# Kernel optimization log

Hardware: AMD Instinct MI355X
Metric: run time of the kernel (lower is better)

## Reference

```python
import jax, jax.numpy as jnp
import numpy as np

POOL = 7
IMG_H, IMG_W = 1024, 1024
EPS = 1e-3  # keras BatchNormalization default epsilon


def crop_and_resize(fmap, boxes, ph, pw):
    # TF tf.image.crop_and_resize (bilinear), box_indices == batch index of each roi.
    # fmap: [B,H,W,C], boxes: [B,N,4] normalized (y1,x1,y2,x2) -> [B,N,ph,pw,C]
    B, H, W, C = fmap.shape
    y1, x1, y2, x2 = jnp.split(boxes, 4, axis=-1)  # each [B,N,1]
    fy = jnp.arange(ph, dtype=boxes.dtype) / (ph - 1)
    fx = jnp.arange(pw, dtype=boxes.dtype) / (pw - 1)
    ys = (y1 + (y2 - y1) * fy) * (H - 1)  # [B,N,ph]
    xs = (x1 + (x2 - x1) * fx) * (W - 1)  # [B,N,pw]
    y0 = jnp.floor(ys)
    x0 = jnp.floor(xs)
    wy = (ys - y0)[:, :, :, None, None]  # [B,N,ph,1,1]
    wx = (xs - x0)[:, :, None, :, None]  # [B,N,1,pw,1]
    y0i = jnp.clip(y0.astype(jnp.int32), 0, H - 1)
    y1i = jnp.clip(y0i + 1, 0, H - 1)
    x0i = jnp.clip(x0.astype(jnp.int32), 0, W - 1)
    x1i = jnp.clip(x0i + 1, 0, W - 1)
    b = jnp.arange(B)[:, None, None, None]
    yi0 = y0i[:, :, :, None]; yi1 = y1i[:, :, :, None]   # [B,N,ph,1]
    xi0 = x0i[:, :, None, :]; xi1 = x1i[:, :, None, :]   # [B,N,1,pw]
    v00 = fmap[b, yi0, xi0]  # [B,N,ph,pw,C]
    v01 = fmap[b, yi0, xi1]
    v10 = fmap[b, yi1, xi0]
    v11 = fmap[b, yi1, xi1]
    top = v00 + (v01 - v00) * wx
    bot = v10 + (v11 - v10) * wx
    return top + (bot - top) * wy


def pyramid_roi_align(rois, fmaps, pool):
    # rois are stop-gradient in the original layer
    rois = jax.lax.stop_gradient(rois)
    y1, x1, y2, x2 = jnp.split(rois, 4, axis=-1)
    h = y2 - y1
    w = x2 - x1
    scale = 256.0 / np.sqrt(float(IMG_H * IMG_W))
    lvl = jnp.log2(jnp.maximum(jnp.sqrt(h * w), 1e-9) / scale)
    lvl = jnp.clip(4 + jnp.round(lvl).astype(jnp.int32), 2, 5)[..., 0]  # [B,N]
    B, N = rois.shape[:2]
    C = fmaps[0].shape[-1]
    out = jnp.zeros((B, N, pool, pool, C), fmaps[0].dtype)
    for i, fm in enumerate(fmaps):  # levels 2..5, fixed small loop
        sel = (lvl == i + 2)[:, :, None, None, None]
        out = jnp.where(sel, crop_and_resize(fm, rois, pool, pool), out)
    return out


def bn_train(x, gamma, beta):
    # keras BatchNorm with training=True: biased batch stats over all axes but channel
    m = x.mean(axis=(0, 1))
    v = x.var(axis=(0, 1))
    return (x - m) * jax.lax.rsqrt(v + EPS) * gamma + beta


def setup_inputs() -> dict:
    key = jax.random.key(0)
    ks = jax.random.split(key, 12)
    B, N, C, F = 2, 1000, 256, 1024
    # rois: valid boxes, sizes spanning all pyramid levels
    tl = jax.random.uniform(ks[0], (B, N, 2), jnp.float32, 0.0, 0.6)
    sz = jax.random.uniform(ks[1], (B, N, 2), jnp.float32, 0.02, 0.4)
    br = jnp.minimum(tl + sz, 1.0)
    rois = jnp.concatenate([tl[..., :1], tl[..., 1:], br[..., :1], br[..., 1:]], axis=-1)
    s = 0.02
    return {
        "rois": rois,
        "p2": jax.random.normal(ks[2], (B, 256, 256, C), jnp.float32),
        "p3": jax.random.normal(ks[3], (B, 128, 128, C), jnp.float32),
        "p4": jax.random.normal(ks[4], (B, 64, 64, C), jnp.float32),
        "p5": jax.random.normal(ks[5], (B, 32, 32, C), jnp.float32),
        "conv1_w": jax.random.normal(ks[6], (POOL, POOL, C, F), jnp.float32) * s,
        "conv1_b": jnp.zeros((F,), jnp.float32),
        "bn1_g": jnp.ones((F,), jnp.float32),
        "bn1_b": jnp.zeros((F,), jnp.float32),
        "conv2_w": jax.random.normal(ks[7], (F, F), jnp.float32) * s,
        "conv2_b": jnp.zeros((F,), jnp.float32),
        "bn2_g": jnp.ones((F,), jnp.float32),
        "bn2_b": jnp.zeros((F,), jnp.float32),
        "cls_w": jax.random.normal(ks[8], (F, 2), jnp.float32) * s,
        "cls_b": jnp.zeros((2,), jnp.float32),
        "delta_w": jax.random.normal(ks[9], (F, 8), jnp.float32) * s,
        "delta_b": jnp.zeros((8,), jnp.float32),
    }


def reference(rois, p2, p3, p4, p5, conv1_w, conv1_b, bn1_g, bn1_b,
              conv2_w, conv2_b, bn2_g, bn2_b, cls_w, cls_b, delta_w, delta_b):
    B, N = rois.shape[:2]
    n_classes = cls_w.shape[-1]
    pooled = pyramid_roi_align(rois, (p2, p3, p4, p5), POOL)  # [B,N,7,7,C]
    # Conv2D(F,(7,7),'valid') on a 7x7 input == full contraction over (h,w,c)
    x = jnp.einsum('bnhwc,hwcf->bnf', pooled, conv1_w) + conv1_b
    x = jax.nn.relu(bn_train(x, bn1_g, bn1_b))
    x = x @ conv2_w + conv2_b  # 1x1 conv == dense
    shared = jax.nn.relu(bn_train(x, bn2_g, bn2_b))  # [B,N,F]
    logits = shared @ cls_w + cls_b                  # [B,N,n_classes]
    probs = jax.nn.softmax(logits, axis=-1)
    deltas = (shared @ delta_w + delta_b).reshape(B, N, n_classes, 4)
    return logits, probs, deltas
```

## Files before the change

kernel.cpp:

```cpp
#include <hip/hip_runtime.h>
#include <hip/hip_bf16.h>

#define NB     2
#define NROI   1000
#define CIN    256
#define FDIM   1024
#define M_ROWS 2000
#define K1     12544
#define EPSBN  1e-3f
#define MN     (M_ROWS * FDIM)

typedef short bf16x8 __attribute__((ext_vector_type(8)));
typedef float f32x4  __attribute__((ext_vector_type(4)));

__device__ __forceinline__ void gld_lds16(const void* g, void* l) {
  __builtin_amdgcn_global_load_lds((const __attribute__((address_space(1))) char*)g,
                                   (__attribute__((address_space(3))) char*)l, 16, 0, 0);
}

__global__ void transpose_to_bf16(const float* __restrict__ W,
                                  __hip_bfloat16* __restrict__ WT,
                                  int K, int N) {
  __shared__ float tile[32][33];
  int k0 = blockIdx.x * 32, n0 = blockIdx.y * 32;
  int t = threadIdx.x;
  int j = t & 31;
  for (int i = t >> 5; i < 32; i += 8)
    tile[i][j] = W[(size_t)(k0 + i) * N + n0 + j];
  __syncthreads();
  int k = t & 31;
  for (int n = t >> 5; n < 32; n += 8)
    WT[(size_t)(n0 + n) * K + k0 + k] = __float2bfloat16(tile[k][n]);
}

__global__ void roi_align_kernel(const float* __restrict__ rois,
                                 const float* __restrict__ p2,
                                 const float* __restrict__ p3,
                                 const float* __restrict__ p4,
                                 const float* __restrict__ p5,
                                 __hip_bfloat16* __restrict__ pooled) {
  int idx = blockIdx.x;
  int pos = idx % 49;
  int rn  = idx / 49;
  int n = rn % NROI, b = rn / NROI;
  int py = pos / 7, px = pos % 7;

  const float* roi = rois + (size_t)(b * NROI + n) * 4;
  float y1 = roi[0], x1 = roi[1], y2 = roi[2], x2 = roi[3];
  float h = y2 - y1, w = x2 - x1;
  float lvl = log2f(fmaxf(sqrtf(h * w), 1e-9f) * 4.0f);
  int li = 4 + (int)rintf(lvl);
  li = min(max(li, 2), 5) - 2;

  const float* fm; int H;
  switch (li) {
    case 0:  fm = p2; H = 256; break;
    case 1:  fm = p3; H = 128; break;
    case 2:  fm = p4; H = 64;  break;
    default: fm = p5; H = 32;  break;
  }
  int W = H;

  float fy = (float)py / 6.0f, fx = (float)px / 6.0f;
  float ys = (y1 + (y2 - y1) * fy) * (float)(H - 1);
  float xs = (x1 + (x2 - x1) * fx) * (float)(W - 1);
  float y0f = floorf(ys), x0f = floorf(xs);
  float wy = ys - y0f, wx = xs - x0f;
  int y0 = min(max((int)y0f, 0), H - 1);
  int x0 = min(max((int)x0f, 0), W - 1);
  int y1i = min(y0 + 1, H - 1);
  int x1i = min(x0 + 1, W - 1);

  size_t base = (size_t)b * H * W * CIN;
  const float* p00 = fm + base + ((size_t)y0 * W + x0) * CIN;
  const float* p01 = fm + base + ((size_t)y0 * W + x1i) * CIN;
  const float* p10 = fm + base + ((size_t)y1i * W + x0) * CIN;
  const float* p11 = fm + base + ((size_t)y1i * W + x1i) * CIN;

  int c = threadIdx.x;
  float v00 = p00[c], v01 = p01[c], v10 = p10[c], v11 = p11[c];
  float top = v00 + (v01 - v00) * wx;
  float bot = v10 + (v11 - v10) * wx;
  float val = top + (bot - top) * wy;
  pooled[(size_t)idx * CIN + c] = __float2bfloat16(val);
}

template<int KSLICES>
__global__ __launch_bounds__(256) void gemm128(const short* __restrict__ A,
                                               const short* __restrict__ BT,
                                               float* __restrict__ P,
                                               int M, int N, int K) {
  __shared__ short As[128 * 32];
  __shared__ short Bs[128 * 32];

  int nwg = gridDim.x;
  int bid = blockIdx.x;
  int cpx = nwg >> 3;
  int wg = (bid & 7) * cpx + (bid >> 3);

  int MT = (M + 127) >> 7;
  int NT = N >> 7;
  int ks   = wg / (MT * NT);
  int tile = wg % (MT * NT);
  int tm = tile % MT, tn = tile / MT;
  int m0 = tm * 128, n0 = tn * 128;
  int Kc = K / KSLICES;
  int kb = ks * Kc;

  int t = threadIdx.x;
  int lane = t & 63, wid = t >> 6;
  int wr = wid >> 1, wc = wid & 1;

  int q0 = wid * 64 + lane;
  int q1 = 256 + q0;
  int as0 = (q0 & 3) * 8, as1 = (q1 & 3) * 8;
  int ar0 = min(m0 + (q0 >> 2), M - 1);
  int ar1 = min(m0 + (q1 >> 2), M - 1);
  const short* Ag0 = A + (size_t)ar0 * K + kb + as0;
  const short* Ag1 = A + (size_t)ar1 * K + kb + as1;
  const short* Bg0 = BT + (size_t)(n0 + (q0 >> 2)) * K + kb + as0;
  const short* Bg1 = BT + (size_t)(n0 + (q1 >> 2)) * K + kb + as1;
  short* Asb0 = As + wid * 512;
  short* Asb1 = As + 2048 + wid * 512;
  short* Bsb0 = Bs + wid * 512;
  short* Bsb1 = Bs + 2048 + wid * 512;

  int lrow = lane & 15, lk = (lane >> 4) * 8;
  const short* Ar = As + (wr * 64 + lrow) * 32 + lk;
  const short* Br = Bs + (wc * 64 + lrow) * 32 + lk;

  f32x4 acc[4][4] = {};

  for (int k0 = 0; k0 < Kc; k0 += 32) {
    __syncthreads();
    gld_lds16(Ag0 + k0, Asb0);
    gld_lds16(Ag1 + k0, Asb1);
    gld_lds16(Bg0 + k0, Bsb0);
    gld_lds16(Bg1 + k0, Bsb1);
    __syncthreads();

    bf16x8 af[4], bfr[4];
#pragma unroll
    for (int i = 0; i < 4; i++) {
      af[i]  = *(const bf16x8*)(Ar + i * 512);
      bfr[i] = *(const bf16x8*)(Br + i * 512);
    }
#pragma unroll
    for (int mi = 0; mi < 4; mi++)
#pragma unroll
      for (int ni = 0; ni < 4; ni++)
        acc[mi][ni] = __builtin_amdgcn_mfma_f32_16x16x32_bf16(af[mi], bfr[ni], acc[mi][ni], 0, 0, 0);
  }

  float* Pb = P + (size_t)ks * M * N;
  int crow = (lane >> 4) * 4, ccol = lane & 15;
#pragma unroll
  for (int mi = 0; mi < 4; mi++) {
    int rb = m0 + wr * 64 + mi * 16 + crow;
#pragma unroll
    for (int ni = 0; ni < 4; ni++) {
      int col = n0 + wc * 64 + ni * 16 + ccol;
#pragma unroll
      for (int r = 0; r < 4; r++) {
        int row = rb + r;
        if (row < M) Pb[(size_t)row * N + col] = acc[mi][ni][r];
      }
    }
  }
}

template<int KS>
__global__ void reduce_bias(const float* __restrict__ P, const float* __restrict__ bias,
                            float* __restrict__ X, int mn, int N) {
  int i4 = blockIdx.x * blockDim.x + threadIdx.x;
  if (i4 * 4 >= mn) return;
  f32x4 s = *(const f32x4*)(P + (size_t)i4 * 4);
#pragma unroll
  for (int c = 1; c < KS; c++)
    s = s + *(const f32x4*)(P + (size_t)c * mn + i4 * 4);
  int col = (i4 * 4) & (N - 1);
  s = s + *(const f32x4*)(bias + col);
  *(f32x4*)(X + (size_t)i4 * 4) = s;
}

__global__ void bn_stats(const float* __restrict__ X, float* __restrict__ stats, int M) {
  int t = threadIdx.x;
  float s0 = 0, s1 = 0, s2 = 0, s3 = 0;
  float q0 = 0, q1 = 0, q2 = 0, q3 = 0;
  for (int r = blockIdx.x; r < M; r += gridDim.x) {
    const float* row = X + (size_t)r * FDIM;
    float v0 = row[t], v1 = row[t + 256], v2 = row[t + 512], v3 = row[t + 768];
    s0 += v0; s1 += v1; s2 += v2; s3 += v3;
    q0 += v0 * v0; q1 += v1 * v1; q2 += v2 * v2; q3 += v3 * v3;
  }
  atomicAdd(&stats[t], s0);        atomicAdd(&stats[t + 256], s1);
  atomicAdd(&stats[t + 512], s2);  atomicAdd(&stats[t + 768], s3);
  atomicAdd(&stats[FDIM + t], q0);       atomicAdd(&stats[FDIM + t + 256], q1);
  atomicAdd(&stats[FDIM + t + 512], q2); atomicAdd(&stats[FDIM + t + 768], q3);
}

template <bool BF16OUT>
__global__ void bn_norm_relu(const float* __restrict__ X, const float* __restrict__ stats,
                             const float* __restrict__ g, const float* __restrict__ bta,
                             __hip_bfloat16* __restrict__ obf, float* __restrict__ of32,
                             int M) {
  int idx = blockIdx.x * blockDim.x + threadIdx.x;
  if (idx >= M * FDIM) return;
  int f = idx & (FDIM - 1);
  float inv_m = 1.0f / (float)M;
  float mean = stats[f] * inv_m;
  float var = stats[FDIM + f] * inv_m - mean * mean;
  float xn = (X[idx] - mean) * rsqrtf(var + EPSBN) * g[f] + bta[f];
  xn = fmaxf(xn, 0.0f);
  if (BF16OUT) obf[idx] = __float2bfloat16(xn);
  else         of32[idx] = xn;
}

__global__ void heads_kernel(const float* __restrict__ S,
                             const float* __restrict__ cls_w, const float* __restrict__ cls_b,
                             const float* __restrict__ dw, const float* __restrict__ db,
                             float* __restrict__ out) {
  int row = blockIdx.x * 4 + (threadIdx.x >> 6);
  int lane = threadIdx.x & 63;
  if (row >= M_ROWS) return;
  const float* srow = S + (size_t)row * FDIM;
  float a[10];
#pragma unroll
  for (int j = 0; j < 10; j++) a[j] = 0.0f;
  for (int k = lane; k < FDIM; k += 64) {
    float v = srow[k];
    a[0] += v * cls_w[k * 2 + 0];
    a[1] += v * cls_w[k * 2 + 1];
#pragma unroll
    for (int j = 0; j < 8; j++) a[2 + j] += v * dw[k * 8 + j];
  }
#pragma unroll
  for (int j = 0; j < 10; j++)
    for (int o = 32; o > 0; o >>= 1) a[j] += __shfl_xor(a[j], o, 64);
  if (lane == 0) {
    float l0 = a[0] + cls_b[0], l1 = a[1] + cls_b[1];
    out[row * 2 + 0] = l0;
    out[row * 2 + 1] = l1;
    float mx = fmaxf(l0, l1);
    float e0 = expf(l0 - mx), e1 = expf(l1 - mx);
    float inv = 1.0f / (e0 + e1);
    out[4000 + row * 2 + 0] = e0 * inv;
    out[4000 + row * 2 + 1] = e1 * inv;
#pragma unroll
    for (int j = 0; j < 8; j++) out[8000 + row * 8 + j] = a[2 + j] + db[j];
  }
}

extern "C" void kernel_launch(void* const* d_in, const int* in_sizes, int n_in,
                              void* d_out, int out_size, void* d_ws, size_t ws_size,
                              hipStream_t stream) {
  const float* rois    = (const float*)d_in[0];
  const float* p2      = (const float*)d_in[1];
  const float* p3      = (const float*)d_in[2];
  const float* p4      = (const float*)d_in[3];
  const float* p5      = (const float*)d_in[4];
  const float* conv1_w = (const float*)d_in[5];
  const float* conv1_b = (const float*)d_in[6];
  const float* bn1_g   = (const float*)d_in[7];
  const float* bn1_b   = (const float*)d_in[8];
  const float* conv2_w = (const float*)d_in[9];
  const float* conv2_b = (const float*)d_in[10];
  const float* bn2_g   = (const float*)d_in[11];
  const float* bn2_b   = (const float*)d_in[12];
  const float* cls_w   = (const float*)d_in[13];
  const float* cls_b   = (const float*)d_in[14];
  const float* delta_w = (const float*)d_in[15];
  const float* delta_b = (const float*)d_in[16];
  float* out = (float*)d_out;

  char* ws = (char*)d_ws;
  size_t off = 0;
  __hip_bfloat16* pooled = (__hip_bfloat16*)(ws + off); off += (size_t)M_ROWS * K1 * 2;
  __hip_bfloat16* w1t    = (__hip_bfloat16*)(ws + off); off += (size_t)K1 * FDIM * 2;
  __hip_bfloat16* w2t    = (__hip_bfloat16*)(ws + off); off += (size_t)FDIM * FDIM * 2;
  float* x1              = (float*)(ws + off);          off += (size_t)MN * 4;
  float* stats1          = (float*)(ws + off);          off += 2 * FDIM * 4;
  float* stats2          = (float*)(ws + off);          off += 2 * FDIM * 4;
  char*  Preg            = ws + off;                    off += (size_t)4 * MN * 4;
  float* part1           = (float*)Preg;
  __hip_bfloat16* x1n    = (__hip_bfloat16*)Preg;
  float* x2              = (float*)(Preg + (size_t)MN * 4);
  float* shared_f        = (float*)(Preg + (size_t)2 * MN * 4);

  hipMemsetAsync(stats1, 0, 4 * FDIM * sizeof(float), stream);

  transpose_to_bf16<<<dim3(K1 / 32, FDIM / 32), 256, 0, stream>>>(conv1_w, w1t, K1, FDIM);
  transpose_to_bf16<<<dim3(FDIM / 32, FDIM / 32), 256, 0, stream>>>(conv2_w, w2t, FDIM, FDIM);

  roi_align_kernel<<<NB * NROI * 49, CIN, 0, stream>>>(rois, p2, p3, p4, p5, pooled);

  gemm128<4><<<512, 256, 0, stream>>>((const short*)pooled, (const short*)w1t, part1,
                                      M_ROWS, FDIM, K1);
  reduce_bias<4><<<MN / 1024, 256, 0, stream>>>(part1, conv1_b, x1, MN, FDIM);

  bn_stats<<<400, 256, 0, stream>>>(x1, stats1, M_ROWS);
  bn_norm_relu<true><<<(MN + 255) / 256, 256, 0, stream>>>(
      x1, stats1, bn1_g, bn1_b, x1n, nullptr, M_ROWS);

  gemm128<2><<<256, 256, 0, stream>>>((const short*)x1n, (const short*)w2t, x2,
                                      M_ROWS, FDIM, FDIM);
  reduce_bias<2><<<MN / 1024, 256, 0, stream>>>(x2, conv2_b, x2, MN, FDIM);

  bn_stats<<<400, 256, 0, stream>>>(x2, stats2, M_ROWS);
  bn_norm_relu<false><<<(MN + 255) / 256, 256, 0, stream>>>(
      x2, stats2, bn2_g, bn2_b, nullptr, shared_f, M_ROWS);

  heads_kernel<<<(M_ROWS + 3) / 4, 256, 0, stream>>>(shared_f, cls_w, cls_b, delta_w, delta_b, out);

  (void)in_sizes; (void)n_in; (void)out_size; (void)ws_size;
}
```

Before: 256.8 us.

## Add 8-wave pipelined GEMM and fuse split-K reduce with BN stats and heads

Replaces the first-layer GEMM with a 512-thread kernel. It uses 128x256 tiles, a multi-buffered global-to-LDS async load pipeline with explicit waitcnt and barrier scheduling, and raised priority for the MFMA section. The split-K reduction and bias add are fused with the batch-norm statistics accumulation. The second batch-norm and ReLU are folded into the heads kernel, which removes the intermediate shared-feature buffer. Workspace buffers are aliased more aggressively, which reorders the second weight transpose, and the larger LDS footprint may limit occupancy.

```diff
diff --git a/kernel.cpp b/kernel.cpp
--- a/kernel.cpp
+++ b/kernel.cpp
@@ -86,13 +86,121 @@
 }
 
 template<int KSLICES>
+__global__ __launch_bounds__(512) void gemm8w(const short* __restrict__ A,
+                                              const short* __restrict__ BT,
+                                              float* __restrict__ P,
+                                              int M, int N, int K) {
+  __shared__ short As[4 * 128 * 32];
+  __shared__ short Bs[4 * 256 * 32];
+
+  int nwg = gridDim.x;
+  int bid = blockIdx.x;
+  int cpx = nwg >> 3;
+  int wg = (bid & 7) * cpx + (bid >> 3);
+
+  int MT = (M + 127) >> 7;
+  int NTn = N >> 8;
+  int tiles = MT * NTn;
+  int ks = wg / tiles;
+  int rem = wg % tiles;
+  int tm = rem % MT, tn = rem / MT;
+  int m0 = tm * 128, n0 = tn * 256;
+  int Kc = K / KSLICES;
+  int NT = Kc >> 6;
+  size_t kb = (size_t)ks * Kc;
+
+  int tid = threadIdx.x;
+  int lane = tid & 63, wid = tid >> 6;
+  int wr = wid >> 2, wc = wid & 3;
+
+  int srow = tid >> 2;
+  int g = (tid & 3) ^ (srow & 3);
+  const short* Agb  = A  + (size_t)min(m0 + srow, M - 1) * K + kb + g * 8;
+  const short* Bgb0 = BT + (size_t)(n0 + srow) * K + kb + g * 8;
+  const short* Bgb1 = Bgb0 + (size_t)128 * K;
+  int aoff  = wid * 512;
+  int boff0 = wid * 512;
+  int boff1 = 4096 + wid * 512;
+
+  int lr = lane & 15;
+  int slotoff = ((lane >> 4) ^ (lane & 3)) * 8;
+  const short* Ard = As + (wr * 64 + lr) * 32 + slotoff;
+  const short* Brd = Bs + (wc * 64 + lr) * 32 + slotoff;
+
+  f32x4 acc[4][4] = {};
+
+#define STAGE(s) do {                                                        \
+    int ts_ = (s) >> 1, kh_ = (s) & 1, b_ = ts_ & 1;                         \
+    int ko_ = ts_ * 64 + kh_ * 32;                                           \
+    short* Ad_ = (short*)As + (b_ * 2 + kh_) * 4096 + aoff;                  \
+    short* Bd_ = (short*)Bs + (b_ * 2 + kh_) * 8192;                         \
+    gld_lds16(Agb + ko_, Ad_);                                               \
+    gld_lds16(Bgb0 + ko_, Bd_ + boff0);                                      \
+    gld_lds16(Bgb1 + ko_, Bd_ + boff1);                                      \
+  } while (0)
+
+  STAGE(0); STAGE(1); STAGE(2);
+
+  for (int t = 0; t < NT; ++t) {
+    int b = t & 1;
+#pragma unroll
+    for (int kh = 0; kh < 2; ++kh) {
+      __builtin_amdgcn_sched_barrier(0);
+      if (t < NT - 1)      asm volatile("s_waitcnt vmcnt(6)" ::: "memory");
+      else if (kh == 0)    asm volatile("s_waitcnt vmcnt(3)" ::: "memory");
+      else                 asm volatile("s_waitcnt vmcnt(0)" ::: "memory");
+      __builtin_amdgcn_s_barrier();
+      __builtin_amdgcn_sched_barrier(0);
+
+      const short* Ab = Ard + (b * 2 + kh) * 4096;
+      const short* Bb = Brd + (b * 2 + kh) * 8192;
+      bf16x8 af[4], bf_[4];
+#pragma unroll
+      for (int mi = 0; mi < 4; mi++) af[mi] = *(const bf16x8*)(Ab + mi * 512);
+#pragma unroll
+      for (int ni = 0; ni < 4; ni++) bf_[ni] = *(const bf16x8*)(Bb + ni * 512);
+
+      if (kh == 0) { if (t + 1 < NT) STAGE(2 * t + 3); }
+      else         { if (t + 2 < NT) STAGE(2 * t + 4); }
+
+      __builtin_amdgcn_sched_barrier(0);
+      asm volatile("s_waitcnt lgkmcnt(0)" ::: "memory");
+      __builtin_amdgcn_sched_barrier(0);
+      __builtin_amdgcn_s_setprio(1);
+#pragma unroll
+      for (int mi = 0; mi < 4; mi++)
+#pragma unroll
+        for (int ni = 0; ni < 4; ni++)
+          acc[mi][ni] = __builtin_amdgcn_mfma_f32_16x16x32_bf16(af[mi], bf_[ni], acc[mi][ni], 0, 0, 0);
+      __builtin_amdgcn_s_setprio(0);
+    }
+  }
+#undef STAGE
+
+  float* Pb = P + (size_t)ks * M * N;
+  int crow = (lane >> 4) * 4, ccol = lane & 15;
+#pragma unroll
+  for (int mi = 0; mi < 4; mi++) {
+    int rb = m0 + wr * 64 + mi * 16 + crow;
+#pragma unroll
+    for (int ni = 0; ni < 4; ni++) {
+      int col = n0 + wc * 64 + ni * 16 + ccol;
+#pragma unroll
+      for (int r = 0; r < 4; r++) {
+        int row = rb + r;
+        if (row < M) Pb[(size_t)row * N + col] = acc[mi][ni][r];
+      }
+    }
+  }
+}
+
+template<int KSLICES>
 __global__ __launch_bounds__(256) void gemm128(const short* __restrict__ A,
                                                const short* __restrict__ BT,
                                                float* __restrict__ P,
                                                int M, int N, int K) {
   __shared__ short As[128 * 32];
   __shared__ short Bs[128 * 32];
-
   int nwg = gridDim.x;
   int bid = blockIdx.x;
   int cpx = nwg >> 3;
@@ -169,41 +277,33 @@
   }
 }
 
-template<int KS>
-__global__ void reduce_bias(const float* __restrict__ P, const float* __restrict__ bias,
-                            float* __restrict__ X, int mn, int N) {
-  int i4 = blockIdx.x * blockDim.x + threadIdx.x;
-  if (i4 * 4 >= mn) return;
-  f32x4 s = *(const f32x4*)(P + (size_t)i4 * 4);
-#pragma unroll
-  for (int c = 1; c < KS; c++)
-    s = s + *(const f32x4*)(P + (size_t)c * mn + i4 * 4);
-  int col = (i4 * 4) & (N - 1);
-  s = s + *(const f32x4*)(bias + col);
-  *(f32x4*)(X + (size_t)i4 * 4) = s;
-}
-
-__global__ void bn_stats(const float* __restrict__ X, float* __restrict__ stats, int M) {
+__global__ void reduce_bias_stats(const float* __restrict__ P, const float* __restrict__ bias,
+                                  float* __restrict__ X, float* __restrict__ stats,
+                                  int M, int KS) {
   int t = threadIdx.x;
-  float s0 = 0, s1 = 0, s2 = 0, s3 = 0;
-  float q0 = 0, q1 = 0, q2 = 0, q3 = 0;
+  int col = t * 4;
+  f32x4 bv = *(const f32x4*)(bias + col);
+  f32x4 s = {0, 0, 0, 0}, q = {0, 0, 0, 0};
   for (int r = blockIdx.x; r < M; r += gridDim.x) {
-    const float* row = X + (size_t)r * FDIM;
-    float v0 = row[t], v1 = row[t + 256], v2 = row[t + 512], v3 = row[t + 768];
-    s0 += v0; s1 += v1; s2 += v2; s3 += v3;
-    q0 += v0 * v0; q1 += v1 * v1; q2 += v2 * v2; q3 += v3 * v3;
-  }
-  atomicAdd(&stats[t], s0);        atomicAdd(&stats[t + 256], s1);
-  atomicAdd(&stats[t + 512], s2);  atomicAdd(&stats[t + 768], s3);
-  atomicAdd(&stats[FDIM + t], q0);       atomicAdd(&stats[FDIM + t + 256], q1);
-  atomicAdd(&stats[FDIM + t + 512], q2); atomicAdd(&stats[FDIM + t + 768], q3);
-}
-
-template <bool BF16OUT>
-__global__ void bn_norm_relu(const float* __restrict__ X, const float* __restrict__ stats,
-                             const float* __restrict__ g, const float* __restrict__ bta,
-                             __hip_bfloat16* __restrict__ obf, float* __restrict__ of32,
-                             int M) {
+    size_t base = (size_t)r * FDIM + col;
+    f32x4 v = *(const f32x4*)(P + base);
+    for (int c = 1; c < KS; c++)
+      v = v + *(const f32x4*)(P + (size_t)c * MN + base);
+    v = v + bv;
+    *(f32x4*)(X + base) = v;
+    s = s + v;
+    q = q + v * v;
+  }
+#pragma unroll
+  for (int j = 0; j < 4; j++) {
+    atomicAdd(&stats[col + j], s[j]);
+    atomicAdd(&stats[FDIM + col + j], q[j]);
+  }
+}
+
+__global__ void bn_norm_relu_bf16(const float* __restrict__ X, const float* __restrict__ stats,
+                                  const float* __restrict__ g, const float* __restrict__ bta,
+                                  __hip_bfloat16* __restrict__ obf, int M) {
   int idx = blockIdx.x * blockDim.x + threadIdx.x;
   if (idx >= M * FDIM) return;
   int f = idx & (FDIM - 1);
@@ -211,24 +311,26 @@
   float mean = stats[f] * inv_m;
   float var = stats[FDIM + f] * inv_m - mean * mean;
   float xn = (X[idx] - mean) * rsqrtf(var + EPSBN) * g[f] + bta[f];
-  xn = fmaxf(xn, 0.0f);
-  if (BF16OUT) obf[idx] = __float2bfloat16(xn);
-  else         of32[idx] = xn;
-}
-
-__global__ void heads_kernel(const float* __restrict__ S,
-                             const float* __restrict__ cls_w, const float* __restrict__ cls_b,
-                             const float* __restrict__ dw, const float* __restrict__ db,
-                             float* __restrict__ out) {
+  obf[idx] = __float2bfloat16(fmaxf(xn, 0.0f));
+}
+
+__global__ void heads_bn(const float* __restrict__ X2, const float* __restrict__ stats,
+                         const float* __restrict__ gg, const float* __restrict__ bb,
+                         const float* __restrict__ cls_w, const float* __restrict__ cls_b,
+                         const float* __restrict__ dw, const float* __restrict__ db,
+                         float* __restrict__ out) {
   int row = blockIdx.x * 4 + (threadIdx.x >> 6);
   int lane = threadIdx.x & 63;
   if (row >= M_ROWS) return;
-  const float* srow = S + (size_t)row * FDIM;
+  const float* xrow = X2 + (size_t)row * FDIM;
+  float inv_m = 1.0f / (float)M_ROWS;
   float a[10];
 #pragma unroll
   for (int j = 0; j < 10; j++) a[j] = 0.0f;
   for (int k = lane; k < FDIM; k += 64) {
-    float v = srow[k];
+    float mean = stats[k] * inv_m;
+    float var = stats[FDIM + k] * inv_m - mean * mean;
+    float v = fmaxf((xrow[k] - mean) * rsqrtf(var + EPSBN) * gg[k] + bb[k], 0.0f);
     a[0] += v * cls_w[k * 2 + 0];
     a[1] += v * cls_w[k * 2 + 1];
 #pragma unroll
@@ -277,40 +379,36 @@
   size_t off = 0;
   __hip_bfloat16* pooled = (__hip_bfloat16*)(ws + off); off += (size_t)M_ROWS * K1 * 2;
   __hip_bfloat16* w1t    = (__hip_bfloat16*)(ws + off); off += (size_t)K1 * FDIM * 2;
-  __hip_bfloat16* w2t    = (__hip_bfloat16*)(ws + off); off += (size_t)FDIM * FDIM * 2;
-  float* x1              = (float*)(ws + off);          off += (size_t)MN * 4;
   float* stats1          = (float*)(ws + off);          off += 2 * FDIM * 4;
   float* stats2          = (float*)(ws + off);          off += 2 * FDIM * 4;
-  char*  Preg            = ws + off;                    off += (size_t)4 * MN * 4;
+  char*  Preg            = ws + off;                    off += (size_t)5 * MN * 4;
   float* part1           = (float*)Preg;
-  __hip_bfloat16* x1n    = (__hip_bfloat16*)Preg;
-  float* x2              = (float*)(Preg + (size_t)MN * 4);
-  float* shared_f        = (float*)(Preg + (size_t)2 * MN * 4);
+  float* x1              = (float*)Preg;
+  __hip_bfloat16* x1n    = (__hip_bfloat16*)(Preg + (size_t)MN * 4);
+  __hip_bfloat16* w2t    = (__hip_bfloat16*)(Preg + (size_t)2 * MN * 4);
+  float* part2           = (float*)(Preg + (size_t)3 * MN * 4);
+  float* x2              = part2;
 
   hipMemsetAsync(stats1, 0, 4 * FDIM * sizeof(float), stream);
 
   transpose_to_bf16<<<dim3(K1 / 32, FDIM / 32), 256, 0, stream>>>(conv1_w, w1t, K1, FDIM);
-  transpose_to_bf16<<<dim3(FDIM / 32, FDIM / 32), 256, 0, stream>>>(conv2_w, w2t, FDIM, FDIM);
 
   roi_align_kernel<<<NB * NROI * 49, CIN, 0, stream>>>(rois, p2, p3, p4, p5, pooled);
 
-  gemm128<4><<<512, 256, 0, stream>>>((const short*)pooled, (const short*)w1t, part1,
-                                      M_ROWS, FDIM, K1);
-  reduce_bias<4><<<MN / 1024, 256, 0, stream>>>(part1, conv1_b, x1, MN, FDIM);
-
-  bn_stats<<<400, 256, 0, stream>>>(x1, stats1, M_ROWS);
-  bn_norm_relu<true><<<(MN + 255) / 256, 256, 0, stream>>>(
-      x1, stats1, bn1_g, bn1_b, x1n, nullptr, M_ROWS);
-
-  gemm128<2><<<256, 256, 0, stream>>>((const short*)x1n, (const short*)w2t, x2,
+  gemm8w<4><<<256, 512, 0, stream>>>((const short*)pooled, (const short*)w1t, part1,
+                                     M_ROWS, FDIM, K1);
+  reduce_bias_stats<<<256, 256, 0, stream>>>(part1, conv1_b, x1, stats1, M_ROWS, 4);
+
+  bn_norm_relu_bf16<<<(MN + 255) / 256, 256, 0, stream>>>(x1, stats1, bn1_g, bn1_b, x1n, M_ROWS);
+
+  transpose_to_bf16<<<dim3(FDIM / 32, FDIM / 32), 256, 0, stream>>>(conv2_w, (__hip_bfloat16*)w2t, FDIM, FDIM);
+
+  gemm128<2><<<256, 256, 0, stream>>>((const short*)x1n, (const short*)w2t, part2,
                                       M_ROWS, FDIM, FDIM);
-  reduce_bias<2><<<MN / 1024, 256, 0, stream>>>(x2, conv2_b, x2, MN, FDIM);
-
-  bn_stats<<<400, 256, 0, stream>>>(x2, stats2, M_ROWS);
-  bn_norm_relu<false><<<(MN + 255) / 256, 256, 0, stream>>>(
-      x2, stats2, bn2_g, bn2_b, nullptr, shared_f, M_ROWS);
-
-  heads_kernel<<<(M_ROWS + 3) / 4, 256, 0, stream>>>(shared_f, cls_w, cls_b, delta_w, delta_b, out);
+  reduce_bias_stats<<<256, 256, 0, stream>>>(part2, conv2_b, x2, stats2, M_ROWS, 2);
+
+  heads_bn<<<(M_ROWS + 3) / 4, 256, 0, stream>>>(x2, stats2, bn2_g, bn2_b,
+                                                 cls_w, cls_b, delta_w, delta_b, out);
 
   (void)in_sizes; (void)n_in; (void)out_size; (void)ws_size;
 }
```

New measurement: 250.1 us. 2.6% less time.
